# Kernel optimization log

Measured on AMD Instinct MI355X. Metric: run time of the kernel, lower is better.

## Reference

```python
import jax, jax.numpy as jnp
import numpy as np

N_HEADS = 16
NEG_INF = -1e30


def setup_inputs() -> dict:
    key = jax.random.key(0)
    ks = jax.random.split(key, 5)
    B, S, D = 2, 2048, 2048
    scale_w = 1.0 / np.sqrt(D)  # keep activations well-scaled
    return {
        "x": jax.random.normal(ks[0], (B, S, D), dtype=jnp.float32),
        "Wq": jax.random.normal(ks[1], (D, D), dtype=jnp.float32) * scale_w,
        "Wk": jax.random.normal(ks[2], (D, D), dtype=jnp.float32) * scale_w,
        "Wv": jax.random.normal(ks[3], (D, D), dtype=jnp.float32) * scale_w,
        "Wo": jax.random.normal(ks[4], (D, D), dtype=jnp.float32) * scale_w,
    }


def reference(x, Wq, Wk, Wv, Wo):
    # Blocked flash attention with online softmax is exactly causal softmax
    # attention; express it directly.
    B, S, D = x.shape
    H = N_HEADS
    dk = D // H
    scale = 1.0 / np.sqrt(dk)

    def heads(w):
        return (x @ w).reshape(B, S, H, dk)

    q = heads(Wq)  # [B,S,H,dk]
    k = heads(Wk)
    v = heads(Wv)

    scores = jnp.einsum("bqhd,bkhd->bhqk", q, k) * scale  # [B,H,S,S]
    causal = jnp.tril(jnp.ones((S, S), dtype=bool))
    scores = jnp.where(causal, scores, NEG_INF)
    p = jax.nn.softmax(scores, axis=-1)
    o = jnp.einsum("bhqk,bkhd->bqhd", p, v).reshape(B, S, D)
    return o @ Wo
```

## Files before the change

kernel.cpp:

```cpp
#include <hip/hip_runtime.h>
#include <hip/hip_bf16.h>

typedef short s16x8 __attribute__((ext_vector_type(8)));
typedef float f32x4 __attribute__((ext_vector_type(4)));
typedef unsigned short u16x4 __attribute__((ext_vector_type(4)));

#define MFMA16(a, b, c) __builtin_amdgcn_mfma_f32_16x16x32_bf16((a), (b), (c), 0, 0, 0)

__device__ __forceinline__ unsigned short f32_to_bf16(float f) {
  unsigned int u = __builtin_bit_cast(unsigned int, f);
  u += 0x7FFFu + ((u >> 16) & 1u);
  return (unsigned short)(u >> 16);
}

__device__ __forceinline__ void glds16(const unsigned short* g, unsigned short* l) {
  __builtin_amdgcn_global_load_lds(
      (const __attribute__((address_space(1))) void*)g,
      (__attribute__((address_space(3))) void*)l, 16, 0, 0);
}

#define BAR() { asm volatile("" ::: "memory"); __builtin_amdgcn_s_barrier(); \
                __builtin_amdgcn_sched_barrier(0); }

__global__ void cvt_bf16_k(const float* __restrict__ in, unsigned short* __restrict__ out, int n4) {
  int i = blockIdx.x * 256 + threadIdx.x;
  if (i >= n4) return;
  float4 f = ((const float4*)in)[i];
  u16x4 o;
  o.x = f32_to_bf16(f.x); o.y = f32_to_bf16(f.y);
  o.z = f32_to_bf16(f.z); o.w = f32_to_bf16(f.w);
  ((u16x4*)out)[i] = o;
}

__global__ void cvt_t4_k(const float* __restrict__ Wq, const float* __restrict__ Wk,
                         const float* __restrict__ Wv, const float* __restrict__ Wo,
                         unsigned short* __restrict__ outQKV, unsigned short* __restrict__ outO,
                         int D) {
  int z = blockIdx.z;
  const float* in = (z == 0) ? Wq : (z == 1) ? Wk : (z == 2) ? Wv : Wo;
  unsigned short* out = (z < 3) ? (outQKV + (size_t)z * D * D) : outO;
  __shared__ float tile[32][33];
  int tx = threadIdx.x;
  int nt = D >> 5;
  int bx = blockIdx.x % nt;
  int by = blockIdx.x / nt;
  int r = tx >> 3, c4 = (tx & 7) * 4;
  int k0 = by * 32, n0 = bx * 32;
  float4 f = *(const float4*)(in + (size_t)(k0 + r) * D + n0 + c4);
  tile[r][c4 + 0] = f.x; tile[r][c4 + 1] = f.y;
  tile[r][c4 + 2] = f.z; tile[r][c4 + 3] = f.w;
  __syncthreads();
  u16x4 o;
  o.x = f32_to_bf16(tile[c4 + 0][r]);
  o.y = f32_to_bf16(tile[c4 + 1][r]);
  o.z = f32_to_bf16(tile[c4 + 2][r]);
  o.w = f32_to_bf16(tile[c4 + 3][r]);
  *(u16x4*)(out + (size_t)(n0 + r) * D + k0 + c4) = o;
}

template <int OUTF32>
__global__ __launch_bounds__(512, 2) void gemm256(
    const unsigned short* __restrict__ A, const unsigned short* __restrict__ Bt,
    void* __restrict__ Cv, int M, int N, int K, int ldc) {
  __shared__ unsigned short Asl[4][128 * 64];
  __shared__ unsigned short Bsl[4][128 * 64];
  int t = threadIdx.x, lane = t & 63, w = t >> 6;
  int r16 = lane & 15, kg = lane >> 4;
  int wm = w >> 2, wn = w & 3;
  int nbn = N >> 8;
  int bm = blockIdx.x / nbn, bn = blockIdx.x % nbn;
  const unsigned short* Ag = A + (size_t)bm * 256 * K;
  const unsigned short* Bg = Bt + (size_t)bn * 256 * K;

  const unsigned short* asrc[2][2];
  const unsigned short* bsrc[2][2];
  int doff[2];
#pragma unroll
  for (int i = 0; i < 2; ++i) {
    int c = i * 512 + t;
    int r = c >> 3, s = c & 7;
    int col = (s ^ (r & 7)) * 8;
#pragma unroll
    for (int h = 0; h < 2; ++h) {
      asrc[h][i] = Ag + (size_t)(h * 128 + r) * K + col;
      bsrc[h][i] = Bg + (size_t)(h * 128 + r) * K + col;
    }
    doff[i] = (i * 512 + (t & ~63)) * 8;
  }

#define HTA(tt, h) { int sl_ = (((tt) & 1) << 1) + (h); int ko_ = (tt) * 64; \
    glds16(asrc[h][0] + ko_, &Asl[sl_][doff[0]]); \
    glds16(asrc[h][1] + ko_, &Asl[sl_][doff[1]]); }
#define HTB(tt, h) { int sl_ = (((tt) & 1) << 1) + (h); int ko_ = (tt) * 64; \
    glds16(bsrc[h][0] + ko_, &Bsl[sl_][doff[0]]); \
    glds16(bsrc[h][1] + ko_, &Bsl[sl_][doff[1]]); }

  f32x4 acc[8][4] = {};
  int nt = K >> 6;
  HTA(0, 0); HTA(0, 1); HTB(0, 0); HTB(0, 1); HTA(1, 0); HTA(1, 1);
  asm volatile("s_waitcnt vmcnt(4)" ::: "memory");
  __builtin_amdgcn_s_barrier();
  __builtin_amdgcn_sched_barrier(0);

  for (int kt = 0; kt < nt; ++kt) {
    int sA = ((kt & 1) << 1) + wm;
    int sB = ((kt & 1) << 1) + (wn >> 1);
    int rB0 = (wn & 1) * 64;
    s16x8 af[8][2], bq[2][2], bq2[2][2];
    if (kt + 1 < nt) HTB(kt + 1, 0);
#pragma unroll
    for (int mf = 0; mf < 4; ++mf) {
      int rl = mf * 16 + r16;
#pragma unroll
      for (int ks = 0; ks < 2; ++ks)
        af[mf][ks] = *(const s16x8*)&Asl[sA][rl * 64 + (((ks * 4 + kg) ^ (r16 & 7)) * 8)];
    }
#pragma unroll
    for (int nf = 0; nf < 2; ++nf) {
      int rl = rB0 + nf * 16 + r16;
#pragma unroll
      for (int ks = 0; ks < 2; ++ks)
        bq[nf][ks] = *(const s16x8*)&Bsl[sB][rl * 64 + (((ks * 4 + kg) ^ (r16 & 7)) * 8)];
    }
    __builtin_amdgcn_s_setprio(1);
#pragma unroll
    for (int ks = 0; ks < 2; ++ks)
#pragma unroll
      for (int mf = 0; mf < 4; ++mf)
#pragma unroll
        for (int nf = 0; nf < 2; ++nf)
          acc[mf][nf] = MFMA16(af[mf][ks], bq[nf][ks], acc[mf][nf]);
    __builtin_amdgcn_s_setprio(0);
    BAR();
    if (kt + 1 < nt) HTB(kt + 1, 1);
#pragma unroll
    for (int mf = 4; mf < 8; ++mf) {
      int rl = mf * 16 + r16;
#pragma unroll
      for (int ks = 0; ks < 2; ++ks)
        af[mf][ks] = *(const s16x8*)&Asl[sA][rl * 64 + (((ks * 4 + kg) ^ (r16 & 7)) * 8)];
    }
    __builtin_amdgcn_s_setprio(1);
#pragma unroll
    for (int ks = 0; ks < 2; ++ks)
#pragma unroll
      for (int mf = 4; mf < 8; ++mf)
#pragma unroll
        for (int nf = 0; nf < 2; ++nf)
          acc[mf][nf] = MFMA16(af[mf][ks], bq[nf][ks], acc[mf][nf]);
    __builtin_amdgcn_s_setprio(0);
    BAR();
    if (kt + 2 < nt) HTA(kt + 2, 0);
#pragma unroll
    for (int nf = 0; nf < 2; ++nf) {
      int rl = rB0 + (nf + 2) * 16 + r16;
#pragma unroll
      for (int ks = 0; ks < 2; ++ks)
        bq2[nf][ks] = *(const s16x8*)&Bsl[sB][rl * 64 + (((ks * 4 + kg) ^ (r16 & 7)) * 8)];
    }
    __builtin_amdgcn_s_setprio(1);
#pragma unroll
    for (int ks = 0; ks < 2; ++ks)
#pragma unroll
      for (int mf = 0; mf < 4; ++mf)
#pragma unroll
        for (int nf = 0; nf < 2; ++nf)
          acc[mf][nf + 2] = MFMA16(af[mf][ks], bq2[nf][ks], acc[mf][nf + 2]);
    __builtin_amdgcn_s_setprio(0);
    BAR();
    if (kt + 2 < nt) HTA(kt + 2, 1);
    __builtin_amdgcn_s_setprio(1);
#pragma unroll
    for (int ks = 0; ks < 2; ++ks)
#pragma unroll
      for (int mf = 4; mf < 8; ++mf)
#pragma unroll
        for (int nf = 0; nf < 2; ++nf)
          acc[mf][nf + 2] = MFMA16(af[mf][ks], bq2[nf][ks], acc[mf][nf + 2]);
    __builtin_amdgcn_s_setprio(0);
    if (kt + 1 < nt) {
      if (kt + 2 < nt) { asm volatile("s_waitcnt vmcnt(4)" ::: "memory"); }
      else             { asm volatile("s_waitcnt vmcnt(0)" ::: "memory"); }
    }
    BAR();
  }
#undef HTA
#undef HTB
#pragma unroll
  for (int mf = 0; mf < 8; ++mf)
#pragma unroll
    for (int nf = 0; nf < 4; ++nf)
#pragma unroll
      for (int r = 0; r < 4; ++r) {
        int row = bm * 256 + wm * 128 + mf * 16 + kg * 4 + r;
        int col = bn * 256 + wn * 64 + nf * 16 + r16;
        if (OUTF32)
          ((float*)Cv)[(size_t)row * ldc + col] = acc[mf][nf][r];
        else
          ((unsigned short*)Cv)[(size_t)row * ldc + col] = f32_to_bf16(acc[mf][nf][r]);
      }
}

template <int OUTF32>
__global__ __launch_bounds__(512, 2) void gemm3(
    const unsigned short* __restrict__ A, const unsigned short* __restrict__ Bt,
    void* __restrict__ Cv, int M, int N, int K, int ldc) {
  __shared__ unsigned short As[3][256 * 64];
  __shared__ unsigned short Bs[3][128 * 64];
  int t = threadIdx.x, lane = t & 63, w = t >> 6;
  int r16 = lane & 15, kg = lane >> 4;
  int wm = w >> 1, wn = w & 1;
  int nbn = N >> 7;
  int bm = blockIdx.x / nbn, bn = blockIdx.x % nbn;
  const unsigned short* Ag = A + (size_t)bm * 256 * K;
  const unsigned short* Bg = Bt + (size_t)bn * 128 * K;

  const unsigned short* asrc[4];
  const unsigned short* bsrc[2];
  int aoff[4], boff[2];
#pragma unroll
  for (int i = 0; i < 4; ++i) {
    int c = i * 512 + t;
    int row = c >> 3, sl = c & 7;
    asrc[i] = Ag + (size_t)row * K + ((sl ^ (row & 7)) * 8);
    aoff[i] = (i * 512 + (t & ~63)) * 8;
  }
#pragma unroll
  for (int i = 0; i < 2; ++i) {
    int c = i * 512 + t;
    int row = c >> 3, sl = c & 7;
    bsrc[i] = Bg + (size_t)row * K + ((sl ^ (row & 7)) * 8);
    boff[i] = (i * 512 + (t & ~63)) * 8;
  }

  auto STAGE = [&](int bi, int kt2) {
    int k0 = kt2 * 64;
#pragma unroll
    for (int i = 0; i < 4; ++i) glds16(asrc[i] + k0, &As[bi][aoff[i]]);
#pragma unroll
    for (int i = 0; i < 2; ++i) glds16(bsrc[i] + k0, &Bs[bi][boff[i]]);
  };

  f32x4 acc[4][4] = {};
  int nt = K >> 6;
  STAGE(0, 0);
  if (nt > 1) STAGE(1, 1);
  int cur = 0;
  for (int kt = 0; kt < nt; ++kt) {
    if (kt + 1 < nt) {
      asm volatile("s_waitcnt vmcnt(6)" ::: "memory");
    } else {
      asm volatile("s_waitcnt vmcnt(0)" ::: "memory");
    }
    __builtin_amdgcn_s_barrier();
    asm volatile("" ::: "memory");
    if (kt + 2 < nt) {
      int s2 = cur + 2; if (s2 >= 3) s2 -= 3;
      STAGE(s2, kt + 2);
    }
    const unsigned short* Al = As[cur];
    s16x8 af[4][2], bfr[4][2];
#pragma unroll
    for (int mf = 0; mf < 4; ++mf) {
      int row = wm * 64 + mf * 16 + r16;
#pragma unroll
      for (int ks = 0; ks < 2; ++ks)
        af[mf][ks] = *(const s16x8*)&Al[row * 64 + (((ks * 4 + kg) ^ (row & 7)) * 8)];
    }
#pragma unroll
    for (int nf = 0; nf < 4; ++nf) {
      int row = wn * 64 + nf * 16 + r16;
#pragma unroll
      for (int ks = 0; ks < 2; ++ks)
        bfr[nf][ks] = *(const s16x8*)&Bs[cur][row * 64 + (((ks * 4 + kg) ^ (row & 7)) * 8)];
    }
    __builtin_amdgcn_s_setprio(1);
#pragma unroll
    for (int ks = 0; ks < 2; ++ks)
#pragma unroll
      for (int mf = 0; mf < 4; ++mf)
#pragma unroll
        for (int nf = 0; nf < 4; ++nf)
          acc[mf][nf] = MFMA16(af[mf][ks], bfr[nf][ks], acc[mf][nf]);
    __builtin_amdgcn_s_setprio(0);
    cur = (cur == 2) ? 0 : cur + 1;
  }
#pragma unroll
  for (int mf = 0; mf < 4; ++mf)
#pragma unroll
    for (int nf = 0; nf < 4; ++nf)
#pragma unroll
      for (int r = 0; r < 4; ++r) {
        int row = bm * 256 + wm * 64 + mf * 16 + kg * 4 + r;
        int col = bn * 128 + wn * 64 + nf * 16 + r16;
        if (OUTF32)
          ((float*)Cv)[(size_t)row * ldc + col] = acc[mf][nf][r];
        else
          ((unsigned short*)Cv)[(size_t)row * ldc + col] = f32_to_bf16(acc[mf][nf][r]);
      }
}

__global__ __launch_bounds__(256) void vtr_k(const unsigned short* __restrict__ V,
                                             unsigned short* __restrict__ Vt,
                                             int S, int ld) {
  __shared__ unsigned short T[32 * 128];
  int s0 = blockIdx.x * 32, h = blockIdx.y, b = blockIdx.z;
  int H = gridDim.y;
  int t = threadIdx.x;
  const unsigned short* src = V + (size_t)(b * S + s0) * ld + h * 128;
#pragma unroll
  for (int c = 0; c < 2; ++c) {
    int chunk = c * 256 + t;
    int row = chunk >> 4, slot = chunk & 15;
    glds16(src + (size_t)row * ld + slot * 8, &T[(c * 256 + (t & ~63)) * 8]);
  }
  __syncthreads();
  unsigned short* dst = Vt + ((size_t)(b * H + h) * (S >> 3) + (s0 >> 3)) * 1024;
#pragma unroll
  for (int c = 0; c < 2; ++c) {
    int oc = c * 256 + t;
    int sl = oc >> 7, d = oc & 127;
    s16x8 v;
#pragma unroll
    for (int j = 0; j < 8; ++j) v[j] = (short)T[(sl * 8 + j) * 128 + d];
    *(s16x8*)(dst + (size_t)oc * 8) = v;
  }
}

__global__ __launch_bounds__(512) void attn2_k(
    const unsigned short* __restrict__ Q, const unsigned short* __restrict__ Kx,
    const unsigned short* __restrict__ Vt, unsigned short* __restrict__ O,
    int S, int D, int Bn, int ld) {
  const float scale = 0.08838834764831843f;
  int hb = blockIdx.x;
  int h = hb / Bn, b = hb % Bn;
  int qp = blockIdx.y;
  int NQ = S >> 7;
  int H = D >> 7;
  int t = threadIdx.x, lane = t & 63, w = t >> 6;
  int r16 = lane & 15, kg = lane >> 4;
  const unsigned short* Qb  = Q + (size_t)b * S * ld + h * 128;
  const unsigned short* Kb  = Kx + (size_t)b * S * ld + h * 128;
  const unsigned short* Vtb = Vt + (size_t)(b * H + h) * (S >> 3) * 1024;

  __shared__ unsigned short Kbuf[2][64 * 128];
  __shared__ unsigned short Vbuf[2][64 * 128];
  __shared__ unsigned short Pl[8][16 * 64];

  auto STAGE = [&](int bufi, int kv0) {
    const unsigned short* Ksrc = Kb + (size_t)kv0 * ld;
#pragma unroll
    for (int c = 0; c < 2; ++c) {
      int chunk = c * 512 + t;
      int row = chunk >> 4, slot = chunk & 15;
      glds16(Ksrc + (size_t)row * ld + ((slot ^ (row & 7)) * 8),
             &Kbuf[bufi][(c * 512 + (t & ~63)) * 8]);
    }
    const unsigned short* Vsrc = Vtb + (size_t)(kv0 >> 3) * 1024;
#pragma unroll
    for (int c = 0; c < 2; ++c) {
      int chunk = c * 512 + t;
      glds16(Vsrc + (size_t)chunk * 8, &Vbuf[bufi][(c * 512 + (t & ~63)) * 8]);
    }
  };

  for (int hf = 0; hf < 2; ++hf) {
    int qt = hf ? (NQ - 1 - qp) : qp;
    int W0 = qt * 128 + w * 16;
    int qg = W0 + r16;
    s16x8 qf[4];
#pragma unroll
    for (int ks = 0; ks < 4; ++ks)
      qf[ks] = *(const s16x8*)(Qb + (size_t)qg * ld + ks * 32 + kg * 8);
    f32x4 oacc[8] = {};
    float m_st = -1e30f, l_st = 0.f;
    int nt = (qt + 1) * 2;
    int cur = 0;
    STAGE(0, 0);
    __syncthreads();
    for (int it = 0; it < nt; ++it) {
      int kv0 = it * 64;
      if (it + 1 < nt) STAGE(cur ^ 1, (it + 1) * 64);
      const unsigned short* Kl = Kbuf[cur];
      const unsigned short* Vl = Vbuf[cur];
      if (kv0 <= W0 + 15) {
        f32x4 st4[4];
        __builtin_amdgcn_s_setprio(1);
#pragma unroll
        for (int kf = 0; kf < 4; ++kf) {
          f32x4 s = {};
#pragma unroll
          for (int ks = 0; ks < 4; ++ks) {
            int row = kf * 16 + r16;
            s16x8 kfr = *(const s16x8*)&Kl[row * 128 + (((ks * 4 + kg) ^ (row & 7)) * 8)];
            s = MFMA16(kfr, qf[ks], s);
          }
          st4[kf] = s;
        }
        __builtin_amdgcn_s_setprio(0);
        float p[4][4];
        float mx = -1e30f;
#pragma unroll
        for (int kf = 0; kf < 4; ++kf)
#pragma unroll
          for (int r = 0; r < 4; ++r) {
            int kvg = kv0 + kf * 16 + kg * 4 + r;
            float sv = st4[kf][r] * scale;
            sv = (kvg <= qg) ? sv : -1e30f;
            p[kf][r] = sv;
            mx = fmaxf(mx, sv);
          }
        mx = fmaxf(mx, __shfl_xor(mx, 16, 64));
        mx = fmaxf(mx, __shfl_xor(mx, 32, 64));
        float m_new = fmaxf(m_st, mx);
        float alpha = __expf(m_st - m_new);
        float rs = 0.f;
#pragma unroll
        for (int kf = 0; kf < 4; ++kf)
#pragma unroll
          for (int r = 0; r < 4; ++r) {
            float e = __expf(p[kf][r] - m_new);
            p[kf][r] = e;
            rs += e;
          }
        rs += __shfl_xor(rs, 16, 64);
        rs += __shfl_xor(rs, 32, 64);
        l_st = l_st * alpha + rs;
        m_st = m_new;
#pragma unroll
        for (int kf = 0; kf < 4; ++kf) {
          unsigned int lo = (unsigned int)f32_to_bf16(p[kf][0]) | ((unsigned int)f32_to_bf16(p[kf][1]) << 16);
          unsigned int hi = (unsigned int)f32_to_bf16(p[kf][2]) | ((unsigned int)f32_to_bf16(p[kf][3]) << 16);
          int sslot = 2 * kf + (kg >> 1);
          int base = r16 * 64 + ((sslot ^ (r16 & 7)) * 8) + (kg & 1) * 4;
          *(unsigned int*)&Pl[w][base]     = lo;
          *(unsigned int*)&Pl[w][base + 2] = hi;
        }
        asm volatile("s_waitcnt lgkmcnt(0)" ::: "memory");
        __builtin_amdgcn_sched_barrier(0);
        float ar[4];
#pragma unroll
        for (int r = 0; r < 4; ++r) ar[r] = __shfl(alpha, kg * 4 + r, 64);
#pragma unroll
        for (int f = 0; f < 8; ++f)
#pragma unroll
          for (int r = 0; r < 4; ++r) oacc[f][r] *= ar[r];
        __builtin_amdgcn_s_setprio(1);
#pragma unroll
        for (int tt = 0; tt < 2; ++tt) {
          s16x8 pf = *(const s16x8*)&Pl[w][r16 * 64 + (((4 * tt + kg) ^ (r16 & 7)) * 8)];
#pragma unroll
          for (int f = 0; f < 8; ++f) {
            s16x8 vf = *(const s16x8*)&Vl[((4 * tt + kg) * 128 + f * 16 + r16) * 8];
            oacc[f] = MFMA16(pf, vf, oacc[f]);
          }
        }
        __builtin_amdgcn_s_setprio(0);
      }
      __syncthreads();
      cur ^= 1;
    }
    float linv = 1.0f / l_st;
    float lr[4];
#pragma unroll
    for (int r = 0; r < 4; ++r) lr[r] = __shfl(linv, kg * 4 + r, 64);
#pragma unroll
    for (int f = 0; f < 8; ++f)
#pragma unroll
      for (int r = 0; r < 4; ++r) {
        size_t idx = ((size_t)b * S + W0 + kg * 4 + r) * D + h * 128 + f * 16 + r16;
        O[idx] = f32_to_bf16(oacc[f][r] * lr[r]);
      }
  }
}

extern "C" void kernel_launch(void* const* d_in, const int* in_sizes, int n_in,
                              void* d_out, int out_size, void* d_ws, size_t ws_size,
                              hipStream_t stream) {
  const float* x  = (const float*)d_in[0];
  const float* Wq = (const float*)d_in[1];
  const float* Wk = (const float*)d_in[2];
  const float* Wv = (const float*)d_in[3];
  const float* Wo = (const float*)d_in[4];
  const int D = 2048, H = 16;
  const int M = in_sizes[0] / D;
  const int B = 2, S = M / B;
  const int LD = 3 * D;

  unsigned short* xb    = (unsigned short*)d_ws;
  unsigned short* Wqkvt = xb + (size_t)M * D;
  unsigned short* Wot   = Wqkvt + (size_t)3 * D * D;
  unsigned short* QKVb  = Wot + (size_t)D * D;
  unsigned short* Ob    = xb;
  unsigned short* VtA   = Wqkvt;

  int n4 = M * D / 4;
  cvt_bf16_k<<<(n4 + 255) / 256, 256, 0, stream>>>(x, xb, n4);
  int tgrid = (D / 32) * (D / 32);
  cvt_t4_k<<<dim3(tgrid, 1, 4), 256, 0, stream>>>(Wq, Wk, Wv, Wo, Wqkvt, Wot, D);

  gemm256<0><<<(M / 256) * (LD / 256), 512, 0, stream>>>(xb, Wqkvt, QKVb, M, LD, D, LD);

  vtr_k<<<dim3(S / 32, H, B), 256, 0, stream>>>(QKVb + 2 * D, VtA, S, LD);

  attn2_k<<<dim3(H * B, S / 256), 512, 0, stream>>>(QKVb, QKVb + D, VtA, Ob, S, D, B, LD);

  gemm3<1><<<(M / 256) * (D / 128), 512, 0, stream>>>(Ob, Wot, d_out, M, D, D, D);
}
```

Baseline: 304.1 us.

## Use 256x192 QKV GEMM tiles and one query tile per attention block

The QKV projection GEMM moves from 256x256 to 256x192 output tiles, giving 16x32=512 blocks instead of 384 so the grid spreads better over the CUs. B staging is reworked into two 192-row buffers filled in three 64-row chunks. The attention kernel stops pairing a short and a long causal query tile in each block. It launches one block per 128-row query tile, longest first, which doubles the grid and relies on the hardware scheduler to balance the causal work. In exchange the GEMM does more B traffic per FLOP, and the attention kernel loses the explicit load pairing.

Result: slower. 310.8 us (+2.2%).

```diff
diff --git a/kernel.cpp b/kernel.cpp
--- a/kernel.cpp
+++ b/kernel.cpp
@@ -59,21 +59,20 @@
 }
 
 template <int OUTF32>
-__global__ __launch_bounds__(512, 2) void gemm256(
+__global__ __launch_bounds__(512, 2) void gemm192(
     const unsigned short* __restrict__ A, const unsigned short* __restrict__ Bt,
     void* __restrict__ Cv, int M, int N, int K, int ldc) {
   __shared__ unsigned short Asl[4][128 * 64];
-  __shared__ unsigned short Bsl[4][128 * 64];
+  __shared__ unsigned short Bsl[2][192 * 64];
   int t = threadIdx.x, lane = t & 63, w = t >> 6;
   int r16 = lane & 15, kg = lane >> 4;
   int wm = w >> 2, wn = w & 3;
-  int nbn = N >> 8;
+  int nbn = N / 192;
   int bm = blockIdx.x / nbn, bn = blockIdx.x % nbn;
   const unsigned short* Ag = A + (size_t)bm * 256 * K;
-  const unsigned short* Bg = Bt + (size_t)bn * 256 * K;
+  const unsigned short* Bg = Bt + (size_t)bn * 192 * K;
 
   const unsigned short* asrc[2][2];
-  const unsigned short* bsrc[2][2];
   int doff[2];
 #pragma unroll
   for (int i = 0; i < 2; ++i) {
@@ -81,33 +80,32 @@
     int r = c >> 3, s = c & 7;
     int col = (s ^ (r & 7)) * 8;
 #pragma unroll
-    for (int h = 0; h < 2; ++h) {
+    for (int h = 0; h < 2; ++h)
       asrc[h][i] = Ag + (size_t)(h * 128 + r) * K + col;
-      bsrc[h][i] = Bg + (size_t)(h * 128 + r) * K + col;
-    }
     doff[i] = (i * 512 + (t & ~63)) * 8;
   }
+  int brow = t >> 3;
+  const unsigned short* bsrc0 = Bg + (size_t)brow * K + (((t & 7) ^ (brow & 7)) * 8);
+  int bdoff = (t & ~63) * 8;
 
 #define HTA(tt, h) { int sl_ = (((tt) & 1) << 1) + (h); int ko_ = (tt) * 64; \
     glds16(asrc[h][0] + ko_, &Asl[sl_][doff[0]]); \
     glds16(asrc[h][1] + ko_, &Asl[sl_][doff[1]]); }
-#define HTB(tt, h) { int sl_ = (((tt) & 1) << 1) + (h); int ko_ = (tt) * 64; \
-    glds16(bsrc[h][0] + ko_, &Bsl[sl_][doff[0]]); \
-    glds16(bsrc[h][1] + ko_, &Bsl[sl_][doff[1]]); }
-
-  f32x4 acc[8][4] = {};
+#define HTB3(tt, j) { int p_ = (tt) & 1; \
+    glds16(bsrc0 + (size_t)(j) * 64 * K + (tt) * 64, &Bsl[p_][(j) * 4096 + bdoff]); }
+
+  f32x4 acc[8][3] = {};
   int nt = K >> 6;
-  HTA(0, 0); HTA(0, 1); HTB(0, 0); HTB(0, 1); HTA(1, 0); HTA(1, 1);
+  HTA(0, 0); HTA(0, 1); HTB3(0, 0); HTB3(0, 1); HTB3(0, 2); HTA(1, 0); HTA(1, 1);
   asm volatile("s_waitcnt vmcnt(4)" ::: "memory");
   __builtin_amdgcn_s_barrier();
   __builtin_amdgcn_sched_barrier(0);
 
   for (int kt = 0; kt < nt; ++kt) {
     int sA = ((kt & 1) << 1) + wm;
-    int sB = ((kt & 1) << 1) + (wn >> 1);
-    int rB0 = (wn & 1) * 64;
-    s16x8 af[8][2], bq[2][2], bq2[2][2];
-    if (kt + 1 < nt) HTB(kt + 1, 0);
+    const unsigned short* Bl = Bsl[kt & 1];
+    s16x8 af[8][2], bq[2][2], bq2[2];
+    if (kt + 1 < nt) HTB3(kt + 1, 0);
 #pragma unroll
     for (int mf = 0; mf < 4; ++mf) {
       int rl = mf * 16 + r16;
@@ -117,10 +115,10 @@
     }
 #pragma unroll
     for (int nf = 0; nf < 2; ++nf) {
-      int rl = rB0 + nf * 16 + r16;
+      int rl = wn * 48 + nf * 16 + r16;
 #pragma unroll
       for (int ks = 0; ks < 2; ++ks)
-        bq[nf][ks] = *(const s16x8*)&Bsl[sB][rl * 64 + (((ks * 4 + kg) ^ (r16 & 7)) * 8)];
+        bq[nf][ks] = *(const s16x8*)&Bl[rl * 64 + (((ks * 4 + kg) ^ (rl & 7)) * 8)];
     }
     __builtin_amdgcn_s_setprio(1);
 #pragma unroll
@@ -132,7 +130,7 @@
           acc[mf][nf] = MFMA16(af[mf][ks], bq[nf][ks], acc[mf][nf]);
     __builtin_amdgcn_s_setprio(0);
     BAR();
-    if (kt + 1 < nt) HTB(kt + 1, 1);
+    if (kt + 1 < nt) HTB3(kt + 1, 1);
 #pragma unroll
     for (int mf = 4; mf < 8; ++mf) {
       int rl = mf * 16 + r16;
@@ -150,22 +148,20 @@
           acc[mf][nf] = MFMA16(af[mf][ks], bq[nf][ks], acc[mf][nf]);
     __builtin_amdgcn_s_setprio(0);
     BAR();
+    if (kt + 1 < nt) HTB3(kt + 1, 2);
     if (kt + 2 < nt) HTA(kt + 2, 0);
-#pragma unroll
-    for (int nf = 0; nf < 2; ++nf) {
-      int rl = rB0 + (nf + 2) * 16 + r16;
+    {
+      int rl = wn * 48 + 32 + r16;
 #pragma unroll
       for (int ks = 0; ks < 2; ++ks)
-        bq2[nf][ks] = *(const s16x8*)&Bsl[sB][rl * 64 + (((ks * 4 + kg) ^ (r16 & 7)) * 8)];
+        bq2[ks] = *(const s16x8*)&Bl[rl * 64 + (((ks * 4 + kg) ^ (rl & 7)) * 8)];
     }
     __builtin_amdgcn_s_setprio(1);
 #pragma unroll
     for (int ks = 0; ks < 2; ++ks)
 #pragma unroll
       for (int mf = 0; mf < 4; ++mf)
-#pragma unroll
-        for (int nf = 0; nf < 2; ++nf)
-          acc[mf][nf + 2] = MFMA16(af[mf][ks], bq2[nf][ks], acc[mf][nf + 2]);
+        acc[mf][2] = MFMA16(af[mf][ks], bq2[ks], acc[mf][2]);
     __builtin_amdgcn_s_setprio(0);
     BAR();
     if (kt + 2 < nt) HTA(kt + 2, 1);
@@ -174,9 +170,7 @@
     for (int ks = 0; ks < 2; ++ks)
 #pragma unroll
       for (int mf = 4; mf < 8; ++mf)
-#pragma unroll
-        for (int nf = 0; nf < 2; ++nf)
-          acc[mf][nf + 2] = MFMA16(af[mf][ks], bq2[nf][ks], acc[mf][nf + 2]);
+        acc[mf][2] = MFMA16(af[mf][ks], bq2[ks], acc[mf][2]);
     __builtin_amdgcn_s_setprio(0);
     if (kt + 1 < nt) {
       if (kt + 2 < nt) { asm volatile("s_waitcnt vmcnt(4)" ::: "memory"); }
@@ -185,15 +179,15 @@
     BAR();
   }
 #undef HTA
-#undef HTB
+#undef HTB3
 #pragma unroll
   for (int mf = 0; mf < 8; ++mf)
 #pragma unroll
-    for (int nf = 0; nf < 4; ++nf)
+    for (int nf = 0; nf < 3; ++nf)
 #pragma unroll
       for (int r = 0; r < 4; ++r) {
         int row = bm * 256 + wm * 128 + mf * 16 + kg * 4 + r;
-        int col = bn * 256 + wn * 64 + nf * 16 + r16;
+        int col = bn * 192 + wn * 48 + nf * 16 + r16;
         if (OUTF32)
           ((float*)Cv)[(size_t)row * ldc + col] = acc[mf][nf][r];
         else
@@ -334,8 +328,8 @@
   const float scale = 0.08838834764831843f;
   int hb = blockIdx.x;
   int h = hb / Bn, b = hb % Bn;
-  int qp = blockIdx.y;
   int NQ = S >> 7;
+  int qt = NQ - 1 - blockIdx.y;
   int H = D >> 7;
   int t = threadIdx.x, lane = t & 63, w = t >> 6;
   int r16 = lane & 15, kg = lane >> 4;
@@ -364,114 +358,111 @@
     }
   };
 
-  for (int hf = 0; hf < 2; ++hf) {
-    int qt = hf ? (NQ - 1 - qp) : qp;
-    int W0 = qt * 128 + w * 16;
-    int qg = W0 + r16;
-    s16x8 qf[4];
-#pragma unroll
-    for (int ks = 0; ks < 4; ++ks)
-      qf[ks] = *(const s16x8*)(Qb + (size_t)qg * ld + ks * 32 + kg * 8);
-    f32x4 oacc[8] = {};
-    float m_st = -1e30f, l_st = 0.f;
-    int nt = (qt + 1) * 2;
-    int cur = 0;
-    STAGE(0, 0);
+  int W0 = qt * 128 + w * 16;
+  int qg = W0 + r16;
+  s16x8 qf[4];
+#pragma unroll
+  for (int ks = 0; ks < 4; ++ks)
+    qf[ks] = *(const s16x8*)(Qb + (size_t)qg * ld + ks * 32 + kg * 8);
+  f32x4 oacc[8] = {};
+  float m_st = -1e30f, l_st = 0.f;
+  int nt = (qt + 1) * 2;
+  int cur = 0;
+  STAGE(0, 0);
+  __syncthreads();
+  for (int it = 0; it < nt; ++it) {
+    int kv0 = it * 64;
+    if (it + 1 < nt) STAGE(cur ^ 1, (it + 1) * 64);
+    const unsigned short* Kl = Kbuf[cur];
+    const unsigned short* Vl = Vbuf[cur];
+    if (kv0 <= W0 + 15) {
+      f32x4 st4[4];
+      __builtin_amdgcn_s_setprio(1);
+#pragma unroll
+      for (int kf = 0; kf < 4; ++kf) {
+        f32x4 s = {};
+#pragma unroll
+        for (int ks = 0; ks < 4; ++ks) {
+          int row = kf * 16 + r16;
+          s16x8 kfr = *(const s16x8*)&Kl[row * 128 + (((ks * 4 + kg) ^ (row & 7)) * 8)];
+          s = MFMA16(kfr, qf[ks], s);
+        }
+        st4[kf] = s;
+      }
+      __builtin_amdgcn_s_setprio(0);
+      float p[4][4];
+      float mx = -1e30f;
+#pragma unroll
+      for (int kf = 0; kf < 4; ++kf)
+#pragma unroll
+        for (int r = 0; r < 4; ++r) {
+          int kvg = kv0 + kf * 16 + kg * 4 + r;
+          float sv = st4[kf][r] * scale;
+          sv = (kvg <= qg) ? sv : -1e30f;
+          p[kf][r] = sv;
+          mx = fmaxf(mx, sv);
+        }
+      mx = fmaxf(mx, __shfl_xor(mx, 16, 64));
+      mx = fmaxf(mx, __shfl_xor(mx, 32, 64));
+      float m_new = fmaxf(m_st, mx);
+      float alpha = __expf(m_st - m_new);
+      float rs = 0.f;
+#pragma unroll
+      for (int kf = 0; kf < 4; ++kf)
+#pragma unroll
+        for (int r = 0; r < 4; ++r) {
+          float e = __expf(p[kf][r] - m_new);
+          p[kf][r] = e;
+          rs += e;
+        }
+      rs += __shfl_xor(rs, 16, 64);
+      rs += __shfl_xor(rs, 32, 64);
+      l_st = l_st * alpha + rs;
+      m_st = m_new;
+#pragma unroll
+      for (int kf = 0; kf < 4; ++kf) {
+        unsigned int lo = (unsigned int)f32_to_bf16(p[kf][0]) | ((unsigned int)f32_to_bf16(p[kf][1]) << 16);
+        unsigned int hi = (unsigned int)f32_to_bf16(p[kf][2]) | ((unsigned int)f32_to_bf16(p[kf][3]) << 16);
+        int sslot = 2 * kf + (kg >> 1);
+        int base = r16 * 64 + ((sslot ^ (r16 & 7)) * 8) + (kg & 1) * 4;
+        *(unsigned int*)&Pl[w][base]     = lo;
+        *(unsigned int*)&Pl[w][base + 2] = hi;
+      }
+      asm volatile("s_waitcnt lgkmcnt(0)" ::: "memory");
+      __builtin_amdgcn_sched_barrier(0);
+      float ar[4];
+#pragma unroll
+      for (int r = 0; r < 4; ++r) ar[r] = __shfl(alpha, kg * 4 + r, 64);
+#pragma unroll
+      for (int f = 0; f < 8; ++f)
+#pragma unroll
+        for (int r = 0; r < 4; ++r) oacc[f][r] *= ar[r];
+      __builtin_amdgcn_s_setprio(1);
+#pragma unroll
+      for (int tt = 0; tt < 2; ++tt) {
+        s16x8 pf = *(const s16x8*)&Pl[w][r16 * 64 + (((4 * tt + kg) ^ (r16 & 7)) * 8)];
+#pragma unroll
+        for (int f = 0; f < 8; ++f) {
+          s16x8 vf = *(const s16x8*)&Vl[((4 * tt + kg) * 128 + f * 16 + r16) * 8];
+          oacc[f] = MFMA16(pf, vf, oacc[f]);
+        }
+      }
+      __builtin_amdgcn_s_setprio(0);
+    }
     __syncthreads();
-    for (int it = 0; it < nt; ++it) {
-      int kv0 = it * 64;
-      if (it + 1 < nt) STAGE(cur ^ 1, (it + 1) * 64);
-      const unsigned short* Kl = Kbuf[cur];
-      const unsigned short* Vl = Vbuf[cur];
-      if (kv0 <= W0 + 15) {
-        f32x4 st4[4];
-        __builtin_amdgcn_s_setprio(1);
-#pragma unroll
-        for (int kf = 0; kf < 4; ++kf) {
-          f32x4 s = {};
-#pragma unroll
-          for (int ks = 0; ks < 4; ++ks) {
-            int row = kf * 16 + r16;
-            s16x8 kfr = *(const s16x8*)&Kl[row * 128 + (((ks * 4 + kg) ^ (row & 7)) * 8)];
-            s = MFMA16(kfr, qf[ks], s);
-          }
-          st4[kf] = s;
-        }
-        __builtin_amdgcn_s_setprio(0);
-        float p[4][4];
-        float mx = -1e30f;
-#pragma unroll
-        for (int kf = 0; kf < 4; ++kf)
-#pragma unroll
-          for (int r = 0; r < 4; ++r) {
-            int kvg = kv0 + kf * 16 + kg * 4 + r;
-            float sv = st4[kf][r] * scale;
-            sv = (kvg <= qg) ? sv : -1e30f;
-            p[kf][r] = sv;
-            mx = fmaxf(mx, sv);
-          }
-        mx = fmaxf(mx, __shfl_xor(mx, 16, 64));
-        mx = fmaxf(mx, __shfl_xor(mx, 32, 64));
-        float m_new = fmaxf(m_st, mx);
-        float alpha = __expf(m_st - m_new);
-        float rs = 0.f;
-#pragma unroll
-        for (int kf = 0; kf < 4; ++kf)
-#pragma unroll
-          for (int r = 0; r < 4; ++r) {
-            float e = __expf(p[kf][r] - m_new);
-            p[kf][r] = e;
-            rs += e;
-          }
-        rs += __shfl_xor(rs, 16, 64);
-        rs += __shfl_xor(rs, 32, 64);
-        l_st = l_st * alpha + rs;
-        m_st = m_new;
-#pragma unroll
-        for (int kf = 0; kf < 4; ++kf) {
-          unsigned int lo = (unsigned int)f32_to_bf16(p[kf][0]) | ((unsigned int)f32_to_bf16(p[kf][1]) << 16);
-          unsigned int hi = (unsigned int)f32_to_bf16(p[kf][2]) | ((unsigned int)f32_to_bf16(p[kf][3]) << 16);
-          int sslot = 2 * kf + (kg >> 1);
-          int base = r16 * 64 + ((sslot ^ (r16 & 7)) * 8) + (kg & 1) * 4;
-          *(unsigned int*)&Pl[w][base]     = lo;
-          *(unsigned int*)&Pl[w][base + 2] = hi;
-        }
-        asm volatile("s_waitcnt lgkmcnt(0)" ::: "memory");
-        __builtin_amdgcn_sched_barrier(0);
-        float ar[4];
-#pragma unroll
-        for (int r = 0; r < 4; ++r) ar[r] = __shfl(alpha, kg * 4 + r, 64);
-#pragma unroll
-        for (int f = 0; f < 8; ++f)
-#pragma unroll
-          for (int r = 0; r < 4; ++r) oacc[f][r] *= ar[r];
-        __builtin_amdgcn_s_setprio(1);
-#pragma unroll
-        for (int tt = 0; tt < 2; ++tt) {
-          s16x8 pf = *(const s16x8*)&Pl[w][r16 * 64 + (((4 * tt + kg) ^ (r16 & 7)) * 8)];
-#pragma unroll
-          for (int f = 0; f < 8; ++f) {
-            s16x8 vf = *(const s16x8*)&Vl[((4 * tt + kg) * 128 + f * 16 + r16) * 8];
-            oacc[f] = MFMA16(pf, vf, oacc[f]);
-          }
-        }
-        __builtin_amdgcn_s_setprio(0);
-      }
-      __syncthreads();
-      cur ^= 1;
-    }
-    float linv = 1.0f / l_st;
-    float lr[4];
-#pragma unroll
-    for (int r = 0; r < 4; ++r) lr[r] = __shfl(linv, kg * 4 + r, 64);
-#pragma unroll
-    for (int f = 0; f < 8; ++f)
-#pragma unroll
-      for (int r = 0; r < 4; ++r) {
-        size_t idx = ((size_t)b * S + W0 + kg * 4 + r) * D + h * 128 + f * 16 + r16;
-        O[idx] = f32_to_bf16(oacc[f][r] * lr[r]);
-      }
-  }
+    cur ^= 1;
+  }
+  float linv = 1.0f / l_st;
+  float lr[4];
+#pragma unroll
+  for (int r = 0; r < 4; ++r) lr[r] = __shfl(linv, kg * 4 + r, 64);
+#pragma unroll
+  for (int f = 0; f < 8; ++f)
+#pragma unroll
+    for (int r = 0; r < 4; ++r) {
+      size_t idx = ((size_t)b * S + W0 + kg * 4 + r) * D + h * 128 + f * 16 + r16;
+      O[idx] = f32_to_bf16(oacc[f][r] * lr[r]);
+    }
 }
 
 extern "C" void kernel_launch(void* const* d_in, const int* in_sizes, int n_in,
@@ -499,11 +490,11 @@
   int tgrid = (D / 32) * (D / 32);
   cvt_t4_k<<<dim3(tgrid, 1, 4), 256, 0, stream>>>(Wq, Wk, Wv, Wo, Wqkvt, Wot, D);
 
-  gemm256<0><<<(M / 256) * (LD / 256), 512, 0, stream>>>(xb, Wqkvt, QKVb, M, LD, D, LD);
+  gemm192<0><<<(M / 256) * (LD / 192), 512, 0, stream>>>(xb, Wqkvt, QKVb, M, LD, D, LD);
 
   vtr_k<<<dim3(S / 32, H, B), 256, 0, stream>>>(QKVb + 2 * D, VtA, S, LD);
 
-  attn2_k<<<dim3(H * B, S / 256), 512, 0, stream>>>(QKVb, QKVb + D, VtA, Ob, S, D, B, LD);
+  attn2_k<<<dim3(H * B, S / 128), 512, 0, stream>>>(QKVb, QKVb + D, VtA, Ob, S, D, B, LD);
 
   gemm3<1><<<(M / 256) * (D / 128), 512, 0, stream>>>(Ob, Wot, d_out, M, D, D, D);
 }
```
